# Kernel tuning notes

Measured on AMD Instinct MI355X. Metric: run time of the kernel, lower is better.

The kernel has to match this reference:

```python
import jax, jax.numpy as jnp
import numpy as np

B, S, D = 16, 2048, 128
NEG = -1000000000.0


def setup_inputs() -> dict:
    key = jax.random.key(0)
    kq, kk, kv = jax.random.split(key, 3)
    q = jax.random.normal(kq, (B, S, D), dtype=jnp.float32)
    k = jax.random.normal(kk, (B, S, D), dtype=jnp.float32)
    v = jax.random.normal(kv, (B, S, D), dtype=jnp.float32)
    # causal mask: True entries are masked out (filled with -1e9)
    mask = jnp.broadcast_to(
        jnp.triu(jnp.ones((S, S), dtype=bool), k=1)[None, :, :], (B, S, S)
    )
    return {"q": q, "k": k, "v": v, "mask": mask}


def reference(q, k, v, mask):
    # attn = q @ k^T / sqrt(d_k), masked_fill, softmax over keys, attn @ v
    scale = jnp.sqrt(jnp.asarray(D, dtype=q.dtype))
    attn = jnp.einsum("bqd,bkd->bqk", q, k) / scale
    attn = jnp.where(mask, jnp.asarray(NEG, dtype=attn.dtype), attn)
    attn = jax.nn.softmax(attn, axis=2)
    out = jnp.einsum("bqk,bkd->bqd", attn, v)
    return (out, attn)
```

## Files before the change

### kernel.cpp

```cpp
#include <hip/hip_runtime.h>

#define B_ 16
#define S_ 2048
#define D_ 128

typedef __attribute__((ext_vector_type(8))) short bf16x8;
typedef __attribute__((ext_vector_type(4))) float f32x4;
typedef __attribute__((ext_vector_type(16))) float f32x16;
typedef __attribute__((ext_vector_type(2))) unsigned int u32x2;
typedef __attribute__((ext_vector_type(4))) unsigned int u32x4;

__device__ __forceinline__ unsigned short f2bf(float f) {
    unsigned int u = __builtin_bit_cast(unsigned int, f);
    u += 0x7fff + ((u >> 16) & 1);
    return (unsigned short)(u >> 16);
}

__device__ __forceinline__ void gload16(const void* g, void* l) {
    __builtin_amdgcn_global_load_lds(
        (const __attribute__((address_space(1))) void*)g,
        (__attribute__((address_space(3))) void*)l, 16, 0, 0);
}

#define WAITV(n) asm volatile("s_waitcnt vmcnt(" #n ")" ::: "memory")

__global__ __launch_bounds__(256, 4)
void conv_kv(const float* __restrict__ kg, const float* __restrict__ vg,
             char* __restrict__ kws, char* __restrict__ vws)
{
    __shared__ float lt[64 * 132];
    const int bid = blockIdx.x;
    const int tid = threadIdx.x;
    if (bid < 512) {
        const float* src = kg + ((long)bid << 13);
        char* dst = kws + ((long)bid << 14);
#pragma unroll
        for (int it = 0; it < 4; ++it) {
            const int c = tid + it * 256;
            const int r = c >> 4, j = c & 15;
            f32x4 a = *(const f32x4*)(src + r * 128 + j * 8);
            f32x4 cc = *(const f32x4*)(src + r * 128 + j * 8 + 4);
            u32x4 p;
            p[0] = (unsigned)f2bf(a[0]) | ((unsigned)f2bf(a[1]) << 16);
            p[1] = (unsigned)f2bf(a[2]) | ((unsigned)f2bf(a[3]) << 16);
            p[2] = (unsigned)f2bf(cc[0]) | ((unsigned)f2bf(cc[1]) << 16);
            p[3] = (unsigned)f2bf(cc[2]) | ((unsigned)f2bf(cc[3]) << 16);
            *(u32x4*)(dst + r * 256 + ((j ^ (r & 7)) << 4)) = p;
        }
    } else {
        const int vb = bid - 512;
        const float* src = vg + ((long)vb << 13);
        char* dst = vws + ((long)vb << 14);
#pragma unroll
        for (int it = 0; it < 8; ++it) {
            const int c = tid + it * 256;
            const int r = c >> 5, q = c & 31;
            *(f32x4*)(lt + r * 132 + q * 4) = *(const f32x4*)(src + r * 128 + q * 4);
        }
        __syncthreads();
#pragma unroll
        for (int it = 0; it < 4; ++it) {
            const int c = tid + it * 256;
            const int d = c >> 3, jc = c & 7;
            unsigned short e[8];
#pragma unroll
            for (int ee = 0; ee < 8; ++ee) e[ee] = f2bf(lt[(jc * 8 + ee) * 132 + d]);
            u32x4 p;
            p[0] = (unsigned)e[0] | ((unsigned)e[1] << 16);
            p[1] = (unsigned)e[2] | ((unsigned)e[3] << 16);
            p[2] = (unsigned)e[4] | ((unsigned)e[5] << 16);
            p[3] = (unsigned)e[6] | ((unsigned)e[7] << 16);
            *(u32x4*)(dst + d * 128 + ((jc ^ (d & 7)) << 4)) = p;
        }
    }
}

__device__ __forceinline__ int qtile_of(int b, int t) {
    const int f = (t & 1) ? (t >> 1) : (31 - (t >> 1));
    return (b & 8) ? (31 - f) : f;
}

__global__ __launch_bounds__(256, 2)
void flash_fused(const float* __restrict__ qg, const char* __restrict__ kws,
                 const char* __restrict__ vws,
                 float* __restrict__ outg, float* __restrict__ attng)
{
    __shared__ char lds[65536];

    const int tid = threadIdx.x, lane = tid & 63, w = tid >> 6;
    const int wq = w >> 1, wk = w & 1;
    const int l31 = lane & 31, hi = lane >> 5;
    const int bid = blockIdx.x;
    const int b = bid >> 5;
    const int qt = qtile_of(b, bid & 31);
    const int q0 = qt * 64;
    const int nt = qt + 1;
    const float scale = 0.088388347648318447f;
    const int qrow = q0 + wq * 32 + l31;

    bf16x8 qf[8];
    {
        const float* qr = qg + ((long)b * S_ + qrow) * D_;
#pragma unroll
        for (int km = 0; km < 8; ++km) {
            const int d0 = km * 16 + hi * 8;
            f32x4 a = *(const f32x4*)(qr + d0);
            f32x4 c = *(const f32x4*)(qr + d0 + 4);
            bf16x8 t;
            t[0] = (short)f2bf(a[0]); t[1] = (short)f2bf(a[1]);
            t[2] = (short)f2bf(a[2]); t[3] = (short)f2bf(a[3]);
            t[4] = (short)f2bf(c[0]); t[5] = (short)f2bf(c[1]);
            t[6] = (short)f2bf(c[2]); t[7] = (short)f2bf(c[3]);
            qf[km] = t;
        }
    }
    WAITV(0);

    const char* kb0 = kws + ((long)(b * 32) << 14);
    const char* vb0 = vws + ((long)(b * 32) << 14);
    const int krow = wk * 32 + l31;
    const int krb = krow * 256;
    const int ksw = krow & 7;

#pragma unroll
    for (int it = 0; it < 4; ++it)
        gload16(kb0 + it * 4096 + tid * 16, lds + it * 4096 + tid * 16);

    float sumA = 0.f;
    int buf = 0;
    for (int kt = 0; kt < nt; ++kt) {
        const bool pf = (kt + 1 < nt);
        if (pf) {
            const char* kn = kb0 + ((long)(kt + 1) << 14);
            const int db = (buf ^ 1) * 16384;
#pragma unroll
            for (int it = 0; it < 4; ++it)
                gload16(kn + it * 4096 + tid * 16, lds + db + it * 4096 + tid * 16);
            WAITV(4);
        } else { WAITV(0); }
        __builtin_amdgcn_s_barrier();
        __builtin_amdgcn_sched_barrier(0);

        const char* kbuf = lds + buf * 16384;
        f32x16 a0, a1;
#pragma unroll
        for (int i = 0; i < 16; ++i) { a0[i] = 0.f; a1[i] = 0.f; }
        __builtin_amdgcn_s_setprio(1);
#pragma unroll
        for (int km = 0; km < 8; ++km) {
            bf16x8 kf = *(const bf16x8*)(kbuf + krb + (((km * 2 + hi) ^ ksw) << 4));
            if (km & 1) a1 = __builtin_amdgcn_mfma_f32_32x32x16_bf16(kf, qf[km], a1, 0, 0, 0);
            else        a0 = __builtin_amdgcn_mfma_f32_32x32x16_bf16(kf, qf[km], a0, 0, 0, 0);
        }
        __builtin_amdgcn_s_setprio(0);

        const int kbase = kt * 64 + wk * 32;
#pragma unroll
        for (int r = 0; r < 16; ++r) {
            const int kl = (r & 3) + 8 * (r >> 2) + 4 * hi;
            if (kbase + kl <= qrow) sumA += __expf((a0[r] + a1[r]) * scale);
        }
        __builtin_amdgcn_sched_barrier(0);
        __builtin_amdgcn_s_barrier();
        buf ^= 1;
    }

    sumA += __shfl_xor(sumA, 32, 64);
    float* sums = (float*)lds;
    if (!hi) sums[(wq * 2 + wk) * 32 + l31] = sumA;
    __syncthreads();
    const float invl_l = 1.f / (sums[(wq * 2 + 0) * 32 + l31] + sums[(wq * 2 + 1) * 32 + l31]);
    __syncthreads();

    f32x16 oacc[4];
#pragma unroll
    for (int dt = 0; dt < 4; ++dt)
#pragma unroll
        for (int i = 0; i < 16; ++i) oacc[dt][i] = 0.f;

    float* attn_row = attng + ((long)b * S_ + qrow) * S_;

#pragma unroll
    for (int it = 0; it < 4; ++it)
        gload16(kb0 + it * 4096 + tid * 16, lds + it * 4096 + tid * 16);
#pragma unroll
    for (int it = 0; it < 4; ++it)
        gload16(vb0 + it * 4096 + tid * 16, lds + 32768 + it * 4096 + tid * 16);

    buf = 0;
    for (int kt = 0; kt < nt; ++kt) {
        const bool pf = (kt + 1 < nt);
        if (pf) {
            const char* kn = kb0 + ((long)(kt + 1) << 14);
            const char* vn = vb0 + ((long)(kt + 1) << 14);
            const int db = (buf ^ 1) * 16384;
#pragma unroll
            for (int it = 0; it < 4; ++it)
                gload16(kn + it * 4096 + tid * 16, lds + db + it * 4096 + tid * 16);
#pragma unroll
            for (int it = 0; it < 4; ++it)
                gload16(vn + it * 4096 + tid * 16, lds + 32768 + db + it * 4096 + tid * 16);
        }
        if (kt == 0) { if (pf) { WAITV(8); } else { WAITV(0); } }
        else         { if (pf) { WAITV(12); } else { WAITV(4); } }
        __builtin_amdgcn_s_barrier();
        __builtin_amdgcn_sched_barrier(0);

        const char* kbuf = lds + buf * 16384;
        const char* vbuf = lds + 32768 + buf * 16384;

        f32x16 a0, a1;
#pragma unroll
        for (int i = 0; i < 16; ++i) { a0[i] = 0.f; a1[i] = 0.f; }
        __builtin_amdgcn_s_setprio(1);
#pragma unroll
        for (int km = 0; km < 8; ++km) {
            bf16x8 kf = *(const bf16x8*)(kbuf + krb + (((km * 2 + hi) ^ ksw) << 4));
            if (km & 1) a1 = __builtin_amdgcn_mfma_f32_32x32x16_bf16(kf, qf[km], a1, 0, 0, 0);
            else        a0 = __builtin_amdgcn_mfma_f32_32x32x16_bf16(kf, qf[km], a0, 0, 0, 0);
        }
        __builtin_amdgcn_s_setprio(0);

        const int kbase = kt * 64 + wk * 32;
        unsigned W[8], PW[8];
#pragma unroll
        for (int i = 0; i < 8; ++i) {
            const int r0 = 2 * i;
            const int kl0 = (r0 & 3) + 8 * (r0 >> 2) + 4 * hi;
            const float p0 = (kbase + kl0 > qrow) ? 0.f : __expf((a0[r0] + a1[r0]) * scale);
            const float p1 = (kbase + kl0 + 1 > qrow) ? 0.f : __expf((a0[r0 + 1] + a1[r0 + 1]) * scale);
            W[i] = (unsigned)f2bf(p0) | ((unsigned)f2bf(p1) << 16);
        }
#pragma unroll
        for (int i = 0; i < 8; ++i)
            PW[i] = (unsigned)__shfl_xor((int)W[i], 32, 64);

        bf16x8 pa[2];
        u32x4 frs[2];
#pragma unroll
        for (int kc = 0; kc < 2; ++kc) {
            u32x4 fr;
            fr[0] = hi ? PW[kc * 4 + 2] : W[kc * 4 + 0];
            fr[1] = hi ? PW[kc * 4 + 3] : W[kc * 4 + 1];
            fr[2] = hi ? W[kc * 4 + 2] : PW[kc * 4 + 0];
            fr[3] = hi ? W[kc * 4 + 3] : PW[kc * 4 + 1];
            frs[kc] = fr;
            pa[kc] = __builtin_bit_cast(bf16x8, fr);
        }

        __builtin_amdgcn_s_setprio(1);
#pragma unroll
        for (int dt = 0; dt < 4; ++dt) {
            const int d = dt * 32 + l31;
            const int rowb = d * 128;
            const int sw = (d & 7) << 4;
#pragma unroll
            for (int kc = 0; kc < 2; ++kc) {
                const int jc = wk * 4 + kc * 2 + hi;
                bf16x8 vf = *(const bf16x8*)(vbuf + rowb + ((jc << 4) ^ sw));
                oacc[dt] = __builtin_amdgcn_mfma_f32_32x32x16_bf16(pa[kc], vf, oacc[dt], 0, 0, 0);
            }
        }
        __builtin_amdgcn_s_setprio(0);

        float* arow = attn_row + kbase;
#pragma unroll
        for (int kc = 0; kc < 2; ++kc) {
            const u32x4 fr = frs[kc];
            f32x4 s0, s1;
            s0[0] = __builtin_bit_cast(float, fr[0] << 16) * invl_l;
            s0[1] = __builtin_bit_cast(float, fr[0] & 0xffff0000u) * invl_l;
            s0[2] = __builtin_bit_cast(float, fr[1] << 16) * invl_l;
            s0[3] = __builtin_bit_cast(float, fr[1] & 0xffff0000u) * invl_l;
            s1[0] = __builtin_bit_cast(float, fr[2] << 16) * invl_l;
            s1[1] = __builtin_bit_cast(float, fr[2] & 0xffff0000u) * invl_l;
            s1[2] = __builtin_bit_cast(float, fr[3] << 16) * invl_l;
            s1[3] = __builtin_bit_cast(float, fr[3] & 0xffff0000u) * invl_l;
            *(f32x4*)(arow + kc * 16 + hi * 8) = s0;
            *(f32x4*)(arow + kc * 16 + hi * 8 + 4) = s1;
        }
        __builtin_amdgcn_sched_barrier(0);
        __builtin_amdgcn_s_barrier();
        buf ^= 1;
    }

    __syncthreads();
    float* red = (float*)lds;
    if (wk) {
#pragma unroll
        for (int dt = 0; dt < 4; ++dt)
#pragma unroll
            for (int r = 0; r < 16; ++r) {
                const int qr = (r & 3) + 8 * (r >> 2) + 4 * hi;
                red[wq * 4096 + qr * 128 + dt * 32 + l31] = oacc[dt][r];
            }
    }
    __syncthreads();
    if (!wk) {
        float iv[16];
#pragma unroll
        for (int r = 0; r < 16; ++r) {
            const int qr = (r & 3) + 8 * (r >> 2) + 4 * hi;
            iv[r] = __shfl(invl_l, qr, 64);
        }
        float* ob = outg + ((long)b * S_ + q0 + wq * 32) * D_;
#pragma unroll
        for (int dt = 0; dt < 4; ++dt)
#pragma unroll
            for (int r = 0; r < 16; ++r) {
                const int qr = (r & 3) + 8 * (r >> 2) + 4 * hi;
                ob[(long)qr * D_ + dt * 32 + l31] =
                    (oacc[dt][r] + red[wq * 4096 + qr * 128 + dt * 32 + l31]) * iv[r];
            }
    }

    {
        const int col0 = nt * 64;
        if (col0 < S_) {
            const int nch = (S_ - col0) >> 2;
            const f32x4 z = {0.f, 0.f, 0.f, 0.f};
            float* fb = attng + ((long)b * S_ + q0) * S_ + col0;
            for (int row = w; row < 64; row += 4) {
                float* rb = fb + (long)row * S_;
                for (int c = lane; c < nch; c += 64)
                    *(f32x4*)(rb + c * 4) = z;
            }
        }
    }
}

__global__ __launch_bounds__(256, 2)
void attn_fallback(const float* __restrict__ qg, const float* __restrict__ kg,
                   const float* __restrict__ vg,
                   float* __restrict__ outg, float* __restrict__ attng)
{
    __shared__ unsigned short kT[64 * 128];
    __shared__ unsigned short vT[128 * 64];
    __shared__ unsigned short pT[4][16 * 64];
    const int tid = threadIdx.x, lane = tid & 63, w = tid >> 6;
    const int l15 = lane & 15, l4 = lane >> 4;
    const int bid = blockIdx.x;
    const int b = bid >> 5, qt = 31 - (bid & 31), q0 = qt * 64;
    const float scale = 0.088388347648318447f;
    bf16x8 qf[4];
    {
        const float* qrow = qg + ((long)b * S_ + q0 + w * 16 + l15) * D_;
#pragma unroll
        for (int kk = 0; kk < 4; ++kk) {
            const int d0 = kk * 32 + l4 * 8;
            f32x4 a = *(const f32x4*)(qrow + d0);
            f32x4 c = *(const f32x4*)(qrow + d0 + 4);
            bf16x8 t;
            t[0] = (short)f2bf(a[0]); t[1] = (short)f2bf(a[1]);
            t[2] = (short)f2bf(a[2]); t[3] = (short)f2bf(a[3]);
            t[4] = (short)f2bf(c[0]); t[5] = (short)f2bf(c[1]);
            t[6] = (short)f2bf(c[2]); t[7] = (short)f2bf(c[3]);
            qf[kk] = t;
        }
    }
    float m[4], l[4];
#pragma unroll
    for (int r = 0; r < 4; ++r) { m[r] = -1e30f; l[r] = 0.f; }
    for (int kt = 0; kt <= qt; ++kt) {
        __syncthreads();
        {
            const float* kbase = kg + ((long)b * S_ + kt * 64) * D_;
#pragma unroll
            for (int it = 0; it < 8; ++it) {
                const int c = tid + it * 256, row = c >> 5, dc = c & 31;
                f32x4 a = *(const f32x4*)(kbase + row * D_ + dc * 4);
                u32x2 p;
                p[0] = (unsigned)f2bf(a[0]) | ((unsigned)f2bf(a[1]) << 16);
                p[1] = (unsigned)f2bf(a[2]) | ((unsigned)f2bf(a[3]) << 16);
                *(u32x2*)((char*)kT + row * 256 + ((dc * 8) ^ ((row & 7) << 4))) = p;
            }
        }
        __syncthreads();
        f32x4 acc[4];
#pragma unroll
        for (int n = 0; n < 4; ++n) {
            f32x4 a = {0.f, 0.f, 0.f, 0.f};
            const int krow = n * 16 + l15, rb = krow * 256, swz = (krow & 7) << 4;
#pragma unroll
            for (int kk = 0; kk < 4; ++kk) {
                bf16x8 bf = *(const bf16x8*)((const char*)kT + rb + ((l4 * 16 + kk * 64) ^ swz));
                a = __builtin_amdgcn_mfma_f32_16x16x32_bf16(qf[kk], bf, a, 0, 0, 0);
            }
            acc[n] = a;
        }
        const bool diag = (kt == qt);
        float tm[4] = {-3e38f, -3e38f, -3e38f, -3e38f};
#pragma unroll
        for (int n = 0; n < 4; ++n)
#pragma unroll
            for (int r = 0; r < 4; ++r) {
                float s = acc[n][r] * scale;
                if (diag && (n * 16 + l15 > w * 16 + l4 * 4 + r)) s = -3e38f;
                acc[n][r] = s; tm[r] = fmaxf(tm[r], s);
            }
#pragma unroll
        for (int off = 1; off < 16; off <<= 1)
#pragma unroll
            for (int r = 0; r < 4; ++r) tm[r] = fmaxf(tm[r], __shfl_xor(tm[r], off, 64));
        float sum[4], mn[4];
#pragma unroll
        for (int r = 0; r < 4; ++r) {
            mn[r] = fmaxf(m[r], tm[r]);
            float s0 = 0.f;
#pragma unroll
            for (int n = 0; n < 4; ++n) s0 += __expf(acc[n][r] - mn[r]);
            sum[r] = s0;
        }
#pragma unroll
        for (int off = 1; off < 16; off <<= 1)
#pragma unroll
            for (int r = 0; r < 4; ++r) sum[r] += __shfl_xor(sum[r], off, 64);
#pragma unroll
        for (int r = 0; r < 4; ++r) { l[r] = l[r] * __expf(m[r] - mn[r]) + sum[r]; m[r] = mn[r]; }
    }
    float invl[4];
#pragma unroll
    for (int r = 0; r < 4; ++r) invl[r] = 1.f / l[r];
    f32x4 oacc[8];
#pragma unroll
    for (int n = 0; n < 8; ++n) oacc[n] = (f32x4){0.f, 0.f, 0.f, 0.f};
    float* attn_base = attng + ((long)b * S_ + q0) * S_;
    for (int kt = 0; kt <= qt; ++kt) {
        __syncthreads();
        {
            const float* kbase = kg + ((long)b * S_ + kt * 64) * D_;
#pragma unroll
            for (int it = 0; it < 8; ++it) {
                const int c = tid + it * 256, row = c >> 5, dc = c & 31;
                f32x4 a = *(const f32x4*)(kbase + row * D_ + dc * 4);
                u32x2 p;
                p[0] = (unsigned)f2bf(a[0]) | ((unsigned)f2bf(a[1]) << 16);
                p[1] = (unsigned)f2bf(a[2]) | ((unsigned)f2bf(a[3]) << 16);
                *(u32x2*)((char*)kT + row * 256 + ((dc * 8) ^ ((row & 7) << 4))) = p;
            }
        }
        {
            const float* vbase = vg + ((long)b * S_ + kt * 64) * D_;
#pragma unroll
            for (int it = 0; it < 8; ++it) {
                const int c = tid + it * 256, kr = c & 63, dq = c >> 6;
                f32x4 a = *(const f32x4*)(vbase + kr * D_ + dq * 4);
#pragma unroll
                for (int j = 0; j < 4; ++j) {
                    const int d = dq * 4 + j;
                    *(unsigned short*)((char*)vT + d * 128 + ((kr * 2) ^ ((d & 7) << 4))) = f2bf(a[j]);
                }
            }
        }
        __syncthreads();
        f32x4 acc[4];
#pragma unroll
        for (int n = 0; n < 4; ++n) {
            f32x4 a = {0.f, 0.f, 0.f, 0.f};
            const int krow = n * 16 + l15, rb = krow * 256, swz = (krow & 7) << 4;
#pragma unroll
            for (int kk = 0; kk < 4; ++kk) {
                bf16x8 bf = *(const bf16x8*)((const char*)kT + rb + ((l4 * 16 + kk * 64) ^ swz));
                a = __builtin_amdgcn_mfma_f32_16x16x32_bf16(qf[kk], bf, a, 0, 0, 0);
            }
            acc[n] = a;
        }
        const bool diag = (kt == qt);
#pragma unroll
        for (int n = 0; n < 4; ++n)
#pragma unroll
            for (int r = 0; r < 4; ++r) {
                float s = acc[n][r] * scale;
                if (diag && (n * 16 + l15 > w * 16 + l4 * 4 + r)) s = -3e38f;
                const float p = __expf(s - m[r]) * invl[r];
                attn_base[(long)(w * 16 + l4 * 4 + r) * S_ + kt * 64 + n * 16 + l15] = p;
                const int prow = l4 * 4 + r;
                *(unsigned short*)((char*)&pT[w][0] + prow * 128 + ((n * 32 + l15 * 2) ^ ((prow & 7) << 4))) = f2bf(p);
            }
        asm volatile("s_waitcnt lgkmcnt(0)" ::: "memory");
        __builtin_amdgcn_sched_barrier(0);
        bf16x8 pa[2];
#pragma unroll
        for (int kk = 0; kk < 2; ++kk)
            pa[kk] = *(const bf16x8*)((const char*)&pT[w][0] + l15 * 128 + ((l4 * 16 + kk * 64) ^ ((l15 & 7) << 4)));
#pragma unroll
        for (int n = 0; n < 8; ++n) {
            const int vrow = n * 16 + l15, rb = vrow * 128, swz = (vrow & 7) << 4;
#pragma unroll
            for (int kk = 0; kk < 2; ++kk) {
                bf16x8 bv = *(const bf16x8*)((const char*)vT + rb + ((l4 * 16 + kk * 64) ^ swz));
                oacc[n] = __builtin_amdgcn_mfma_f32_16x16x32_bf16(pa[kk], bv, oacc[n], 0, 0, 0);
            }
        }
    }
    {
        float* obase = outg + ((long)b * S_ + q0 + w * 16) * D_;
#pragma unroll
        for (int n = 0; n < 8; ++n)
#pragma unroll
            for (int r = 0; r < 4; ++r)
                obase[(long)(l4 * 4 + r) * D_ + n * 16 + l15] = oacc[n][r];
    }
    {
        const int col0 = (qt + 1) * 64;
        if (col0 < S_) {
            const int nch = (S_ - col0) >> 2;
            const f32x4 z = {0.f, 0.f, 0.f, 0.f};
            for (int row = w; row < 64; row += 4) {
                float* rbase = attn_base + (long)row * S_ + col0;
                for (int c = lane; c < nch; c += 64)
                    *(f32x4*)(rbase + c * 4) = z;
            }
        }
    }
}

extern "C" void kernel_launch(void* const* d_in, const int* in_sizes, int n_in,
                              void* d_out, int out_size, void* d_ws, size_t ws_size,
                              hipStream_t stream) {
    const float* q = (const float*)d_in[0];
    const float* k = (const float*)d_in[1];
    const float* v = (const float*)d_in[2];
    float* out  = (float*)d_out;
    float* attn = out + (long)B_ * S_ * D_;
    const size_t NEED = 2u * 8388608u;
    if (ws_size >= NEED) {
        char* kws = (char*)d_ws;
        char* vws = kws + 8388608;
        conv_kv<<<dim3(1024), dim3(256), 0, stream>>>(k, v, kws, vws);
        flash_fused<<<dim3(512), dim3(256), 0, stream>>>(q, kws, vws, out, attn);
    } else {
        attn_fallback<<<dim3(512), dim3(256), 0, stream>>>(q, k, v, out, attn);
    }
}
```

Before: 117.4 us.

## Process two K tiles per pass in row-sum loop and XCD-swizzle block mapping

The first (row-sum) pass now loads and processes two 64-row K tiles per barrier pair, using all 64KB of LDS as two double-buffered 32KB slots. This halves the number of barriers and waits in that loop. Block indices in both kernels are remapped so that consecutive tiles of one batch land on the same XCD, which should improve L2 reuse of K/V. The batch-parity rule for reversing the query-tile order changes from bit 3 to bit 1 to keep work balanced. The cost is an extra redundant tile load when the tile count is odd, plus more outstanding memory traffic per stage.

Measured after the change: 113.6 us (median of 3 runs). 3.3% less time.

```diff
diff --git a/kernel.cpp b/kernel.cpp
--- a/kernel.cpp
+++ b/kernel.cpp
@@ -24,14 +24,17 @@
 
 #define WAITV(n) asm volatile("s_waitcnt vmcnt(" #n ")" ::: "memory")
 
+__device__ __forceinline__ int xcd_swz(int raw) { return (raw & 7) * 64 + (raw >> 3); }
+
 __global__ __launch_bounds__(256, 4)
 void conv_kv(const float* __restrict__ kg, const float* __restrict__ vg,
              char* __restrict__ kws, char* __restrict__ vws)
 {
     __shared__ float lt[64 * 132];
-    const int bid = blockIdx.x;
+    const int raw = blockIdx.x;
     const int tid = threadIdx.x;
-    if (bid < 512) {
+    if (raw < 512) {
+        const int bid = xcd_swz(raw);
         const float* src = kg + ((long)bid << 13);
         char* dst = kws + ((long)bid << 14);
 #pragma unroll
@@ -48,7 +51,7 @@
             *(u32x4*)(dst + r * 256 + ((j ^ (r & 7)) << 4)) = p;
         }
     } else {
-        const int vb = bid - 512;
+        const int vb = xcd_swz(raw - 512);
         const float* src = vg + ((long)vb << 13);
         char* dst = vws + ((long)vb << 14);
 #pragma unroll
@@ -77,7 +80,7 @@
 
 __device__ __forceinline__ int qtile_of(int b, int t) {
     const int f = (t & 1) ? (t >> 1) : (31 - (t >> 1));
-    return (b & 8) ? (31 - f) : f;
+    return (b & 1) ? (31 - f) : f;
 }
 
 __global__ __launch_bounds__(256, 2)
@@ -90,7 +93,7 @@
     const int tid = threadIdx.x, lane = tid & 63, w = tid >> 6;
     const int wq = w >> 1, wk = w & 1;
     const int l31 = lane & 31, hi = lane >> 5;
-    const int bid = blockIdx.x;
+    const int bid = xcd_swz(blockIdx.x);
     const int b = bid >> 5;
     const int qt = qtile_of(b, bid & 31);
     const int q0 = qt * 64;
@@ -122,47 +125,64 @@
     const int krb = krow * 256;
     const int ksw = krow & 7;
 
-#pragma unroll
-    for (int it = 0; it < 4; ++it)
-        gload16(kb0 + it * 4096 + tid * 16, lds + it * 4096 + tid * 16);
-
+    const int np = (nt + 1) >> 1;
+    {
+        const char* k1 = kb0 + ((long)((nt > 1) ? 1 : 0) << 14);
+#pragma unroll
+        for (int it = 0; it < 4; ++it)
+            gload16(kb0 + it * 4096 + tid * 16, lds + it * 4096 + tid * 16);
+#pragma unroll
+        for (int it = 0; it < 4; ++it)
+            gload16(k1 + it * 4096 + tid * 16, lds + 16384 + it * 4096 + tid * 16);
+    }
     float sumA = 0.f;
-    int buf = 0;
-    for (int kt = 0; kt < nt; ++kt) {
-        const bool pf = (kt + 1 < nt);
+    int bufA = 0;
+    for (int p = 0; p < np; ++p) {
+        const bool pf = (p + 1 < np);
         if (pf) {
-            const char* kn = kb0 + ((long)(kt + 1) << 14);
-            const int db = (buf ^ 1) * 16384;
+            const int t0 = p * 2 + 2;
+            const int t1 = (t0 + 1 < nt) ? (t0 + 1) : (nt - 1);
+            const char* k0 = kb0 + ((long)t0 << 14);
+            const char* k1 = kb0 + ((long)t1 << 14);
+            const int db = (bufA ^ 1) * 32768;
 #pragma unroll
             for (int it = 0; it < 4; ++it)
-                gload16(kn + it * 4096 + tid * 16, lds + db + it * 4096 + tid * 16);
-            WAITV(4);
+                gload16(k0 + it * 4096 + tid * 16, lds + db + it * 4096 + tid * 16);
+#pragma unroll
+            for (int it = 0; it < 4; ++it)
+                gload16(k1 + it * 4096 + tid * 16, lds + db + 16384 + it * 4096 + tid * 16);
+            WAITV(8);
         } else { WAITV(0); }
         __builtin_amdgcn_s_barrier();
         __builtin_amdgcn_sched_barrier(0);
 
-        const char* kbuf = lds + buf * 16384;
-        f32x16 a0, a1;
-#pragma unroll
-        for (int i = 0; i < 16; ++i) { a0[i] = 0.f; a1[i] = 0.f; }
-        __builtin_amdgcn_s_setprio(1);
-#pragma unroll
-        for (int km = 0; km < 8; ++km) {
-            bf16x8 kf = *(const bf16x8*)(kbuf + krb + (((km * 2 + hi) ^ ksw) << 4));
-            if (km & 1) a1 = __builtin_amdgcn_mfma_f32_32x32x16_bf16(kf, qf[km], a1, 0, 0, 0);
-            else        a0 = __builtin_amdgcn_mfma_f32_32x32x16_bf16(kf, qf[km], a0, 0, 0, 0);
-        }
-        __builtin_amdgcn_s_setprio(0);
-
-        const int kbase = kt * 64 + wk * 32;
-#pragma unroll
-        for (int r = 0; r < 16; ++r) {
-            const int kl = (r & 3) + 8 * (r >> 2) + 4 * hi;
-            if (kbase + kl <= qrow) sumA += __expf((a0[r] + a1[r]) * scale);
+#pragma unroll
+        for (int s = 0; s < 2; ++s) {
+            const int kt = p * 2 + s;
+            if (kt < nt) {
+                const char* kbuf = lds + bufA * 32768 + s * 16384;
+                f32x16 a0, a1;
+#pragma unroll
+                for (int i = 0; i < 16; ++i) { a0[i] = 0.f; a1[i] = 0.f; }
+                __builtin_amdgcn_s_setprio(1);
+#pragma unroll
+                for (int km = 0; km < 8; ++km) {
+                    bf16x8 kf = *(const bf16x8*)(kbuf + krb + (((km * 2 + hi) ^ ksw) << 4));
+                    if (km & 1) a1 = __builtin_amdgcn_mfma_f32_32x32x16_bf16(kf, qf[km], a1, 0, 0, 0);
+                    else        a0 = __builtin_amdgcn_mfma_f32_32x32x16_bf16(kf, qf[km], a0, 0, 0, 0);
+                }
+                __builtin_amdgcn_s_setprio(0);
+                const int kbase = kt * 64 + wk * 32;
+#pragma unroll
+                for (int r = 0; r < 16; ++r) {
+                    const int kl = (r & 3) + 8 * (r >> 2) + 4 * hi;
+                    if (kbase + kl <= qrow) sumA += __expf((a0[r] + a1[r]) * scale);
+                }
+            }
         }
         __builtin_amdgcn_sched_barrier(0);
         __builtin_amdgcn_s_barrier();
-        buf ^= 1;
+        bufA ^= 1;
     }
 
     sumA += __shfl_xor(sumA, 32, 64);
@@ -187,7 +207,7 @@
     for (int it = 0; it < 4; ++it)
         gload16(vb0 + it * 4096 + tid * 16, lds + 32768 + it * 4096 + tid * 16);
 
-    buf = 0;
+    int buf = 0;
     for (int kt = 0; kt < nt; ++kt) {
         const bool pf = (kt + 1 < nt);
         if (pf) {
```

## Replace two-pass softmax with single pass plus attn rescale sweep and XCD swizzle

Applied to the files above, without the earlier changes.

Drops the separate QK^T pass that computed row sums. The sums are now accumulated during the main P·V loop, and unnormalized probabilities are written to attn. A final sweep rereads the causal part of attn and multiplies it by the inverse row sum. Block indices are also remapped across XCDs, and the per-batch tile order pattern changes. This halves the QK MFMA work and K loads, at the cost of an extra read-modify-write over the large attn output.

Result: slower. 139.9 us (+19.1%).

```diff
diff --git a/kernel.cpp b/kernel.cpp
--- a/kernel.cpp
+++ b/kernel.cpp
@@ -24,14 +24,17 @@
 
 #define WAITV(n) asm volatile("s_waitcnt vmcnt(" #n ")" ::: "memory")
 
+__device__ __forceinline__ int xcd_swz(int raw) { return (raw & 7) * 64 + (raw >> 3); }
+
 __global__ __launch_bounds__(256, 4)
 void conv_kv(const float* __restrict__ kg, const float* __restrict__ vg,
              char* __restrict__ kws, char* __restrict__ vws)
 {
     __shared__ float lt[64 * 132];
-    const int bid = blockIdx.x;
+    const int raw = blockIdx.x;
     const int tid = threadIdx.x;
-    if (bid < 512) {
+    if (raw < 512) {
+        const int bid = xcd_swz(raw);
         const float* src = kg + ((long)bid << 13);
         char* dst = kws + ((long)bid << 14);
 #pragma unroll
@@ -48,7 +51,7 @@
             *(u32x4*)(dst + r * 256 + ((j ^ (r & 7)) << 4)) = p;
         }
     } else {
-        const int vb = bid - 512;
+        const int vb = xcd_swz(raw - 512);
         const float* src = vg + ((long)vb << 13);
         char* dst = vws + ((long)vb << 14);
 #pragma unroll
@@ -77,20 +80,20 @@
 
 __device__ __forceinline__ int qtile_of(int b, int t) {
     const int f = (t & 1) ? (t >> 1) : (31 - (t >> 1));
-    return (b & 8) ? (31 - f) : f;
+    return (b & 1) ? (31 - f) : f;
 }
 
 __global__ __launch_bounds__(256, 2)
-void flash_fused(const float* __restrict__ qg, const char* __restrict__ kws,
-                 const char* __restrict__ vws,
-                 float* __restrict__ outg, float* __restrict__ attng)
+void flash_single(const float* __restrict__ qg, const char* __restrict__ kws,
+                  const char* __restrict__ vws,
+                  float* __restrict__ outg, float* __restrict__ attng)
 {
     __shared__ char lds[65536];
 
     const int tid = threadIdx.x, lane = tid & 63, w = tid >> 6;
     const int wq = w >> 1, wk = w & 1;
     const int l31 = lane & 31, hi = lane >> 5;
-    const int bid = blockIdx.x;
+    const int bid = xcd_swz(blockIdx.x);
     const int b = bid >> 5;
     const int qt = qtile_of(b, bid & 31);
     const int q0 = qt * 64;
@@ -122,72 +125,23 @@
     const int krb = krow * 256;
     const int ksw = krow & 7;
 
+    f32x16 oacc[4];
+#pragma unroll
+    for (int dt = 0; dt < 4; ++dt)
+#pragma unroll
+        for (int i = 0; i < 16; ++i) oacc[dt][i] = 0.f;
+    float sumA = 0.f;
+
+    float* attn_row = attng + ((long)b * S_ + qrow) * S_;
+
 #pragma unroll
     for (int it = 0; it < 4; ++it)
         gload16(kb0 + it * 4096 + tid * 16, lds + it * 4096 + tid * 16);
-
-    float sumA = 0.f;
-    int buf = 0;
-    for (int kt = 0; kt < nt; ++kt) {
-        const bool pf = (kt + 1 < nt);
-        if (pf) {
-            const char* kn = kb0 + ((long)(kt + 1) << 14);
-            const int db = (buf ^ 1) * 16384;
-#pragma unroll
-            for (int it = 0; it < 4; ++it)
-                gload16(kn + it * 4096 + tid * 16, lds + db + it * 4096 + tid * 16);
-            WAITV(4);
-        } else { WAITV(0); }
-        __builtin_amdgcn_s_barrier();
-        __builtin_amdgcn_sched_barrier(0);
-
-        const char* kbuf = lds + buf * 16384;
-        f32x16 a0, a1;
-#pragma unroll
-        for (int i = 0; i < 16; ++i) { a0[i] = 0.f; a1[i] = 0.f; }
-        __builtin_amdgcn_s_setprio(1);
-#pragma unroll
-        for (int km = 0; km < 8; ++km) {
-            bf16x8 kf = *(const bf16x8*)(kbuf + krb + (((km * 2 + hi) ^ ksw) << 4));
-            if (km & 1) a1 = __builtin_amdgcn_mfma_f32_32x32x16_bf16(kf, qf[km], a1, 0, 0, 0);
-            else        a0 = __builtin_amdgcn_mfma_f32_32x32x16_bf16(kf, qf[km], a0, 0, 0, 0);
-        }
-        __builtin_amdgcn_s_setprio(0);
-
-        const int kbase = kt * 64 + wk * 32;
-#pragma unroll
-        for (int r = 0; r < 16; ++r) {
-            const int kl = (r & 3) + 8 * (r >> 2) + 4 * hi;
-            if (kbase + kl <= qrow) sumA += __expf((a0[r] + a1[r]) * scale);
-        }
-        __builtin_amdgcn_sched_barrier(0);
-        __builtin_amdgcn_s_barrier();
-        buf ^= 1;
-    }
-
-    sumA += __shfl_xor(sumA, 32, 64);
-    float* sums = (float*)lds;
-    if (!hi) sums[(wq * 2 + wk) * 32 + l31] = sumA;
-    __syncthreads();
-    const float invl_l = 1.f / (sums[(wq * 2 + 0) * 32 + l31] + sums[(wq * 2 + 1) * 32 + l31]);
-    __syncthreads();
-
-    f32x16 oacc[4];
-#pragma unroll
-    for (int dt = 0; dt < 4; ++dt)
-#pragma unroll
-        for (int i = 0; i < 16; ++i) oacc[dt][i] = 0.f;
-
-    float* attn_row = attng + ((long)b * S_ + qrow) * S_;
-
-#pragma unroll
-    for (int it = 0; it < 4; ++it)
-        gload16(kb0 + it * 4096 + tid * 16, lds + it * 4096 + tid * 16);
 #pragma unroll
     for (int it = 0; it < 4; ++it)
         gload16(vb0 + it * 4096 + tid * 16, lds + 32768 + it * 4096 + tid * 16);
 
-    buf = 0;
+    int buf = 0;
     for (int kt = 0; kt < nt; ++kt) {
         const bool pf = (kt + 1 < nt);
         if (pf) {
@@ -229,6 +183,7 @@
             const int kl0 = (r0 & 3) + 8 * (r0 >> 2) + 4 * hi;
             const float p0 = (kbase + kl0 > qrow) ? 0.f : __expf((a0[r0] + a1[r0]) * scale);
             const float p1 = (kbase + kl0 + 1 > qrow) ? 0.f : __expf((a0[r0 + 1] + a1[r0 + 1]) * scale);
+            sumA += p0 + p1;
             W[i] = (unsigned)f2bf(p0) | ((unsigned)f2bf(p1) << 16);
         }
 #pragma unroll
@@ -268,14 +223,14 @@
         for (int kc = 0; kc < 2; ++kc) {
             const u32x4 fr = frs[kc];
             f32x4 s0, s1;
-            s0[0] = __builtin_bit_cast(float, fr[0] << 16) * invl_l;
-            s0[1] = __builtin_bit_cast(float, fr[0] & 0xffff0000u) * invl_l;
-            s0[2] = __builtin_bit_cast(float, fr[1] << 16) * invl_l;
-            s0[3] = __builtin_bit_cast(float, fr[1] & 0xffff0000u) * invl_l;
-            s1[0] = __builtin_bit_cast(float, fr[2] << 16) * invl_l;
-            s1[1] = __builtin_bit_cast(float, fr[2] & 0xffff0000u) * invl_l;
-            s1[2] = __builtin_bit_cast(float, fr[3] << 16) * invl_l;
-            s1[3] = __builtin_bit_cast(float, fr[3] & 0xffff0000u) * invl_l;
+            s0[0] = __builtin_bit_cast(float, fr[0] << 16);
+            s0[1] = __builtin_bit_cast(float, fr[0] & 0xffff0000u);
+            s0[2] = __builtin_bit_cast(float, fr[1] << 16);
+            s0[3] = __builtin_bit_cast(float, fr[1] & 0xffff0000u);
+            s1[0] = __builtin_bit_cast(float, fr[2] << 16);
+            s1[1] = __builtin_bit_cast(float, fr[2] & 0xffff0000u);
+            s1[2] = __builtin_bit_cast(float, fr[3] << 16);
+            s1[3] = __builtin_bit_cast(float, fr[3] & 0xffff0000u);
             *(f32x4*)(arow + kc * 16 + hi * 8) = s0;
             *(f32x4*)(arow + kc * 16 + hi * 8 + 4) = s1;
         }
@@ -284,8 +239,15 @@
         buf ^= 1;
     }
 
+    sumA += __shfl_xor(sumA, 32, 64);
     __syncthreads();
-    float* red = (float*)lds;
+    float* sums   = (float*)lds;
+    float* invl64 = (float*)(lds + 512);
+    float* red    = (float*)(lds + 8192);
+    if (!hi) sums[(wq * 2 + wk) * 32 + l31] = sumA;
+    __syncthreads();
+    const float invl_l = 1.f / (sums[(wq * 2 + 0) * 32 + l31] + sums[(wq * 2 + 1) * 32 + l31]);
+    if (wk == 0 && !hi) invl64[wq * 32 + l31] = invl_l;
     if (wk) {
 #pragma unroll
         for (int dt = 0; dt < 4; ++dt)
@@ -312,6 +274,20 @@
                 ob[(long)qr * D_ + dt * 32 + l31] =
                     (oacc[dt][r] + red[wq * 4096 + qr * 128 + dt * 32 + l31]) * iv[r];
             }
+    }
+
+    {
+        const int nchunk = nt * 16;
+        float* base = attng + ((long)b * S_ + q0 + w * 16) * S_;
+        for (int r = 0; r < 16; ++r) {
+            const float iv = invl64[w * 16 + r];
+            float* ar = base + (long)r * S_;
+            for (int c = lane; c < nchunk; c += 64) {
+                f32x4 v = *(const f32x4*)(ar + c * 4);
+                v[0] *= iv; v[1] *= iv; v[2] *= iv; v[3] *= iv;
+                *(f32x4*)(ar + c * 4) = v;
+            }
+        }
     }
 
     {
@@ -528,7 +504,7 @@
         char* kws = (char*)d_ws;
         char* vws = kws + 8388608;
         conv_kv<<<dim3(1024), dim3(256), 0, stream>>>(k, v, kws, vws);
-        flash_fused<<<dim3(512), dim3(256), 0, stream>>>(q, kws, vws, out, attn);
+        flash_single<<<dim3(512), dim3(256), 0, stream>>>(q, kws, vws, out, attn);
     } else {
         attn_fallback<<<dim3(512), dim3(256), 0, stream>>>(q, k, v, out, attn);
     }
```

## Load K directly to registers in pass one and swizzle blocks across XCDs

Applied to the files above, without the earlier changes.

The first (row-sum) pass no longer stages K tiles through LDS with barriers. Each wave now reads its K fragments straight from global memory into registers, prefetching the next tile while the MFMAs run, which removes the block-wide barriers and LDS round trips. Block indices are remapped so that consecutive work for a batch lands on the same XCD, aiming for better L2 locality in both kernels, and the causal tile-order flip now keys on batch parity. The cost is more registers for the K fragments and uncoalesced 16-byte global reads of the swizzled layout.

Result: no change. 116.6 us (-0.7%).

```diff
diff --git a/kernel.cpp b/kernel.cpp
--- a/kernel.cpp
+++ b/kernel.cpp
@@ -24,14 +24,17 @@
 
 #define WAITV(n) asm volatile("s_waitcnt vmcnt(" #n ")" ::: "memory")
 
+__device__ __forceinline__ int xcd_swz(int raw) { return (raw & 7) * 64 + (raw >> 3); }
+
 __global__ __launch_bounds__(256, 4)
 void conv_kv(const float* __restrict__ kg, const float* __restrict__ vg,
              char* __restrict__ kws, char* __restrict__ vws)
 {
     __shared__ float lt[64 * 132];
-    const int bid = blockIdx.x;
+    const int raw = blockIdx.x;
     const int tid = threadIdx.x;
-    if (bid < 512) {
+    if (raw < 512) {
+        const int bid = xcd_swz(raw);
         const float* src = kg + ((long)bid << 13);
         char* dst = kws + ((long)bid << 14);
 #pragma unroll
@@ -48,7 +51,7 @@
             *(u32x4*)(dst + r * 256 + ((j ^ (r & 7)) << 4)) = p;
         }
     } else {
-        const int vb = bid - 512;
+        const int vb = xcd_swz(raw - 512);
         const float* src = vg + ((long)vb << 13);
         char* dst = vws + ((long)vb << 14);
 #pragma unroll
@@ -77,7 +80,7 @@
 
 __device__ __forceinline__ int qtile_of(int b, int t) {
     const int f = (t & 1) ? (t >> 1) : (31 - (t >> 1));
-    return (b & 8) ? (31 - f) : f;
+    return (b & 1) ? (31 - f) : f;
 }
 
 __global__ __launch_bounds__(256, 2)
@@ -90,7 +93,7 @@
     const int tid = threadIdx.x, lane = tid & 63, w = tid >> 6;
     const int wq = w >> 1, wk = w & 1;
     const int l31 = lane & 31, hi = lane >> 5;
-    const int bid = blockIdx.x;
+    const int bid = xcd_swz(blockIdx.x);
     const int b = bid >> 5;
     const int qt = qtile_of(b, bid & 31);
     const int q0 = qt * 64;
@@ -114,7 +117,6 @@
             qf[km] = t;
         }
     }
-    WAITV(0);
 
     const char* kb0 = kws + ((long)(b * 32) << 14);
     const char* vb0 = vws + ((long)(b * 32) << 14);
@@ -122,50 +124,40 @@
     const int krb = krow * 256;
     const int ksw = krow & 7;
 
-#pragma unroll
-    for (int it = 0; it < 4; ++it)
-        gload16(kb0 + it * 4096 + tid * 16, lds + it * 4096 + tid * 16);
-
     float sumA = 0.f;
-    int buf = 0;
-    for (int kt = 0; kt < nt; ++kt) {
-        const bool pf = (kt + 1 < nt);
-        if (pf) {
-            const char* kn = kb0 + ((long)(kt + 1) << 14);
-            const int db = (buf ^ 1) * 16384;
-#pragma unroll
-            for (int it = 0; it < 4; ++it)
-                gload16(kn + it * 4096 + tid * 16, lds + db + it * 4096 + tid * 16);
-            WAITV(4);
-        } else { WAITV(0); }
-        __builtin_amdgcn_s_barrier();
-        __builtin_amdgcn_sched_barrier(0);
-
-        const char* kbuf = lds + buf * 16384;
-        f32x16 a0, a1;
-#pragma unroll
-        for (int i = 0; i < 16; ++i) { a0[i] = 0.f; a1[i] = 0.f; }
-        __builtin_amdgcn_s_setprio(1);
-#pragma unroll
-        for (int km = 0; km < 8; ++km) {
-            bf16x8 kf = *(const bf16x8*)(kbuf + krb + (((km * 2 + hi) ^ ksw) << 4));
-            if (km & 1) a1 = __builtin_amdgcn_mfma_f32_32x32x16_bf16(kf, qf[km], a1, 0, 0, 0);
-            else        a0 = __builtin_amdgcn_mfma_f32_32x32x16_bf16(kf, qf[km], a0, 0, 0, 0);
-        }
-        __builtin_amdgcn_s_setprio(0);
-
-        const int kbase = kt * 64 + wk * 32;
-#pragma unroll
-        for (int r = 0; r < 16; ++r) {
-            const int kl = (r & 3) + 8 * (r >> 2) + 4 * hi;
-            if (kbase + kl <= qrow) sumA += __expf((a0[r] + a1[r]) * scale);
-        }
-        __builtin_amdgcn_sched_barrier(0);
-        __builtin_amdgcn_s_barrier();
-        buf ^= 1;
+    {
+        bf16x8 kf[8];
+#pragma unroll
+        for (int km = 0; km < 8; ++km)
+            kf[km] = *(const bf16x8*)(kb0 + krb + (((km * 2 + hi) ^ ksw) << 4));
+        for (int kt = 0; kt < nt; ++kt) {
+            f32x16 a0, a1;
+#pragma unroll
+            for (int i = 0; i < 16; ++i) { a0[i] = 0.f; a1[i] = 0.f; }
+            __builtin_amdgcn_s_setprio(1);
+#pragma unroll
+            for (int km = 0; km < 8; ++km) {
+                if (km & 1) a1 = __builtin_amdgcn_mfma_f32_32x32x16_bf16(kf[km], qf[km], a1, 0, 0, 0);
+                else        a0 = __builtin_amdgcn_mfma_f32_32x32x16_bf16(kf[km], qf[km], a0, 0, 0, 0);
+            }
+            __builtin_amdgcn_s_setprio(0);
+            if (kt + 1 < nt) {
+                const char* kn = kb0 + ((long)(kt + 1) << 14);
+#pragma unroll
+                for (int km = 0; km < 8; ++km)
+                    kf[km] = *(const bf16x8*)(kn + krb + (((km * 2 + hi) ^ ksw) << 4));
+            }
+            const int kbase = kt * 64 + wk * 32;
+#pragma unroll
+            for (int r = 0; r < 16; ++r) {
+                const int kl = (r & 3) + 8 * (r >> 2) + 4 * hi;
+                if (kbase + kl <= qrow) sumA += __expf((a0[r] + a1[r]) * scale);
+            }
+        }
     }
 
     sumA += __shfl_xor(sumA, 32, 64);
+    WAITV(0);
     float* sums = (float*)lds;
     if (!hi) sums[(wq * 2 + wk) * 32 + l31] = sumA;
     __syncthreads();
@@ -187,7 +179,7 @@
     for (int it = 0; it < 4; ++it)
         gload16(vb0 + it * 4096 + tid * 16, lds + 32768 + it * 4096 + tid * 16);
 
-    buf = 0;
+    int buf = 0;
     for (int kt = 0; kt < nt; ++kt) {
         const bool pf = (kt + 1 < nt);
         if (pf) {
```
